# Kernel optimization log

Hardware: AMD Instinct MI355X
Metric: run time of the kernel (lower is better)

The kernel has to match this reference:

```python
import jax, jax.numpy as jnp
import numpy as np

V, E, HD, K = 100000, 128, 256, 9
B, T = 128, 512
H = HD // 2  # per-direction hidden size


def setup_inputs() -> dict:
    key = jax.random.key(0)
    ks = jax.random.split(key, 16)
    s = 0.1
    rn = lambda k, shape: jax.random.normal(k, shape, jnp.float32) * s
    sentences = jax.random.randint(ks[0], (B, T), 0, V, dtype=jnp.int32)
    lengths = jax.random.randint(ks[1], (B,), 1, T + 1, dtype=jnp.int32)
    return {
        'sentences': sentences,
        'lengths': lengths,
        'embed': rn(ks[2], (V, E)),
        'Wih_f': rn(ks[3], (4 * H, E)), 'Whh_f': rn(ks[4], (4 * H, H)),
        'bih_f': rn(ks[5], (4 * H,)), 'bhh_f': rn(ks[6], (4 * H,)),
        'Wih_b': rn(ks[7], (4 * H, E)), 'Whh_b': rn(ks[8], (4 * H, H)),
        'bih_b': rn(ks[9], (4 * H,)), 'bhh_b': rn(ks[10], (4 * H,)),
        'W_out': rn(ks[11], (K, HD)), 'b_out': rn(ks[12], (K,)),
        'start_t': rn(ks[13], (K,)), 'end_t': rn(ks[14], (K,)),
        'trans': rn(ks[15], (K, K)),
    }


def _lstm(x, mask, Wih, Whh, bih, bhh, reverse):
    # x: [B,T,E], mask: [B,T] bool. Replicates packed-sequence semantics:
    # state frozen and output zeroed at padding positions (padding is trailing,
    # so reverse=True starts fresh at each sequence's true end).
    Bv, Hv = x.shape[0], Whh.shape[1]
    bias = bih + bhh

    def step(carry, inp):
        h, c = carry
        x_t, m_t = inp  # [B,E], [B,1]
        gates = x_t @ Wih.T + h @ Whh.T + bias  # [B,4H]
        i, f, g, o = jnp.split(gates, 4, axis=-1)  # torch gate order i,f,g,o
        c_new = jax.nn.sigmoid(f) * c + jax.nn.sigmoid(i) * jnp.tanh(g)
        h_new = jax.nn.sigmoid(o) * jnp.tanh(c_new)
        h = jnp.where(m_t, h_new, h)
        c = jnp.where(m_t, c_new, c)
        return (h, c), h * m_t.astype(h.dtype)

    init = (jnp.zeros((Bv, Hv), x.dtype), jnp.zeros((Bv, Hv), x.dtype))
    xs = (jnp.swapaxes(x, 0, 1), jnp.swapaxes(mask, 0, 1)[..., None])
    _, hs = jax.lax.scan(step, init, xs, reverse=reverse)
    return jnp.swapaxes(hs, 0, 1)  # [B,T,H]


def _emissions(sentences, mask, embed, Wih_f, Whh_f, bih_f, bhh_f,
               Wih_b, Whh_b, bih_b, bhh_b, W_out, b_out):
    x = embed[sentences]  # [B,T,E] (dropout is identity at inference)
    hf = _lstm(x, mask, Wih_f, Whh_f, bih_f, bhh_f, reverse=False)
    hb = _lstm(x, mask, Wih_b, Whh_b, bih_b, bhh_b, reverse=True)
    h = jnp.concatenate([hf, hb], axis=-1)  # [B,T,2H]
    return jnp.einsum('btd,kd->btk', h, W_out) + b_out  # [B,T,K]


def _viterbi(em, mask, start_t, end_t, trans):
    # torchcrf-style batched Viterbi decode. em: [B,T,K], mask: [B,T] bool.
    Kv = em.shape[-1]
    ident = jnp.arange(Kv, dtype=jnp.int32)[None]  # identity backpointers for pads
    score0 = start_t[None] + em[:, 0]  # [B,K]

    def step(score, inp):
        em_t, m_t = inp  # [B,K], [B,1]
        cand = score[:, :, None] + trans[None] + em_t[:, None, :]  # [B,K_prev,K_cur]
        new_score = cand.max(axis=1)
        idx = cand.argmax(axis=1).astype(jnp.int32)  # [B,K]
        score = jnp.where(m_t, new_score, score)
        idx = jnp.where(m_t, idx, ident)
        return score, idx

    xs = (jnp.swapaxes(em[:, 1:], 0, 1), jnp.swapaxes(mask[:, 1:], 0, 1)[..., None])
    score, hist = jax.lax.scan(step, score0, xs)  # hist: [T-1,B,K]
    score = score + end_t[None]
    last_tag = jnp.argmax(score, axis=-1).astype(jnp.int32)  # [B]

    def back(tag, idx_t):
        prev = jnp.take_along_axis(idx_t, tag[:, None], axis=1)[:, 0]
        return prev, prev

    _, tags_prev = jax.lax.scan(back, last_tag, hist, reverse=True)  # [T-1,B]
    tags = jnp.swapaxes(jnp.concatenate([tags_prev, last_tag[None]], axis=0), 0, 1)
    return jnp.where(mask, tags, 0), score.max(axis=-1)


def reference(sentences, lengths, embed, Wih_f, Whh_f, bih_f, bhh_f,
              Wih_b, Whh_b, bih_b, bhh_b, W_out, b_out, start_t, end_t, trans):
    mask = jnp.arange(sentences.shape[1])[None] < lengths[:, None]  # [B,T]
    em = _emissions(sentences, mask, embed, Wih_f, Whh_f, bih_f, bhh_f,
                    Wih_b, Whh_b, bih_b, bhh_b, W_out, b_out)
    tags, _ = _viterbi(em, mask, start_t, end_t, trans)
    return tags  # [B,T] int32, padded positions set to 0
```

## Files before the change

### kernel.cpp

```cpp
#include <hip/hip_runtime.h>
#include <cmath>

#define B_  128
#define T_  512
#define E_  128
#define H_  128
#define G4  512
#define K_  9
#define HP  36

__global__ __launch_bounds__(256, 2)
void proj_gemm(const int* __restrict__ sent, const float* __restrict__ embed,
               const float* __restrict__ Wf, const float* __restrict__ Wb,
               const float* __restrict__ bif, const float* __restrict__ bhf,
               const float* __restrict__ bib, const float* __restrict__ bhb,
               float* __restrict__ proj, int t0f, int Tc)
{
  __shared__ __align__(16) float Al[128 * 64];
  __shared__ __align__(16) float Bl[128 * 64];
  const int tid   = threadIdx.x;
  const int ntile = blockIdx.x;
  const int mtile = blockIdx.y;
  const int tpb   = Tc >> 6;
  const int b     = mtile / tpb;
  const int toff  = (mtile - b * tpb) << 6;
  const int dir   = ntile >> 3;
  const int t0    = dir ? (T_ - t0f - Tc) : t0f;
  const float* __restrict__ W = dir ? Wb : Wf;
  const int n0 = (ntile & 7) << 6;

  {
    const int r  = tid & 63;
    const int kc = tid >> 6;
    const int t  = t0 + toff + r;
    const int vid = sent[b * T_ + t];
    const float* arow = embed + (size_t)vid * E_ + kc * 32;
    const float* brow = W + (size_t)(n0 + r) * E_ + kc * 32;
#pragma unroll
    for (int q = 0; q < 8; ++q) {
      float4 av = *(const float4*)(arow + q * 4);
      float4 bv = *(const float4*)(brow + q * 4);
      int k0 = kc * 32 + q * 4;
      Al[(k0 + 0) * 64 + r] = av.x; Al[(k0 + 1) * 64 + r] = av.y;
      Al[(k0 + 2) * 64 + r] = av.z; Al[(k0 + 3) * 64 + r] = av.w;
      Bl[(k0 + 0) * 64 + r] = bv.x; Bl[(k0 + 1) * 64 + r] = bv.y;
      Bl[(k0 + 2) * 64 + r] = bv.z; Bl[(k0 + 3) * 64 + r] = bv.w;
    }
  }
  __syncthreads();

  const int mg = tid & 15, ng = tid >> 4;
  float acc[4][4] = {};
#pragma unroll 8
  for (int k = 0; k < 128; ++k) {
    float4 a  = *(const float4*)&Al[k * 64 + mg * 4];
    float4 bb = *(const float4*)&Bl[k * 64 + ng * 4];
    acc[0][0] += a.x * bb.x; acc[0][1] += a.x * bb.y; acc[0][2] += a.x * bb.z; acc[0][3] += a.x * bb.w;
    acc[1][0] += a.y * bb.x; acc[1][1] += a.y * bb.y; acc[1][2] += a.y * bb.z; acc[1][3] += a.y * bb.w;
    acc[2][0] += a.z * bb.x; acc[2][1] += a.z * bb.y; acc[2][2] += a.z * bb.z; acc[2][3] += a.z * bb.w;
    acc[3][0] += a.w * bb.x; acc[3][1] += a.w * bb.y; acc[3][2] += a.w * bb.z; acc[3][3] += a.w * bb.w;
  }

  const float* bi = dir ? bib : bif;
  const float* bh = dir ? bhb : bhf;
  const int nl = ng * 4;
  float4 bias;
  bias.x = bi[n0 + nl + 0] + bh[n0 + nl + 0];
  bias.y = bi[n0 + nl + 1] + bh[n0 + nl + 1];
  bias.z = bi[n0 + nl + 2] + bh[n0 + nl + 2];
  bias.w = bi[n0 + nl + 3] + bh[n0 + nl + 3];
#pragma unroll
  for (int i = 0; i < 4; ++i) {
    const int tloc = toff + mg * 4 + i;
    float4 o;
    o.x = acc[i][0] + bias.x; o.y = acc[i][1] + bias.y;
    o.z = acc[i][2] + bias.z; o.w = acc[i][3] + bias.w;
    *(float4*)&proj[((size_t)(b * Tc + tloc)) * 1024 + dir * G4 + n0 + nl] = o;
  }
}

__device__ __forceinline__ float fast_rcp(float x) {
  return __builtin_amdgcn_rcpf(x);
}
__device__ __forceinline__ float fast_sig(float x) {
  return fast_rcp(1.f + __expf(-x));
}
__device__ __forceinline__ float fast_tanh(float x) {
  return 2.f * fast_rcp(1.f + __expf(-2.f * x)) - 1.f;
}

__global__ __launch_bounds__(1024)
void lstm_chunk(const float* __restrict__ proj,
                const float* __restrict__ Whf, const float* __restrict__ Whb,
                const int* __restrict__ lengths,
                float* __restrict__ hs,
                float* __restrict__ sh, float* __restrict__ sc,
                int t0f, int Tc, int first)
{
  const int dir = blockIdx.x;
  const int b   = blockIdx.y;
  const int tid = threadIdx.x;
  const int l   = tid & 63;
  const int wv  = tid >> 6;
  const int u   = wv * 8 + (l & 7);
  const int gp  = (l >> 3) & 1;
  const int kq  = l >> 4;
  const int rowA = u + (gp ? 256 : 0);
  const int rowB = rowA + 128;
  const float* __restrict__ Whh = dir ? Whb : Whf;
  __shared__ __align__(16) float h_hist[2][4 * HP];

  float wA[32], wB[32];
  {
    const float* wra = Whh + (size_t)rowA * H_ + kq * 32;
    const float* wrb = Whh + (size_t)rowB * H_ + kq * 32;
#pragma unroll
    for (int k = 0; k < 32; k += 4) {
      float4 va = *(const float4*)(wra + k);
      float4 vb = *(const float4*)(wrb + k);
      wA[k] = va.x; wA[k + 1] = va.y; wA[k + 2] = va.z; wA[k + 3] = va.w;
      wB[k] = vb.x; wB[k + 1] = vb.y; wB[k + 2] = vb.z; wB[k + 3] = vb.w;
    }
  }
#pragma unroll
  for (int k = 0; k < 32; ++k) {
    asm volatile("" : "+v"(wA[k]));
    asm volatile("" : "+v"(wB[k]));
  }

  const int len = lengths[b];
  const int t0  = dir ? (T_ - t0f - Tc) : t0f;
  const float fgp = (float)gp;
  const float kf  = 1.f + fgp;
  float c = 0.f, h_reg = 0.f;
  if (!first) {
    c     = sc[(dir * B_ + b) * H_ + u];
    h_reg = sh[(dir * B_ + b) * H_ + u];
  }
  if (l < 8) h_hist[1][(u >> 5) * HP + (u & 31)] = h_reg;
  __syncthreads();

  const float* projpA = proj + (size_t)b * Tc * 1024 + dir * G4 + rowA;
  const float* projpB = projpA + 128;
  const int tc00 = dir ? (Tc - 1) : 0;
  float pvA = projpA[(size_t)tc00 * 1024];
  float pvB = projpB[(size_t)tc00 * 1024];

  for (int s = 0; s < Tc; ++s) {
    const int tc = dir ? (Tc - 1 - s) : s;
    const int t  = t0 + tc;
    float nvA = 0.f, nvB = 0.f;
    if (s + 1 < Tc) {
      const int tcn = dir ? (Tc - 2 - s) : (s + 1);
      nvA = projpA[(size_t)tcn * 1024];
      nvB = projpB[(size_t)tcn * 1024];
    }
    const float* hp = &h_hist[(s + 1) & 1][kq * HP];
    float a0 = 0.f, a1 = 0.f, a2 = 0.f, a3 = 0.f;
#pragma unroll
    for (int k4 = 0; k4 < 8; ++k4) {
      float4 h4 = *(const float4*)&hp[k4 * 4];
      a0 += wA[4 * k4 + 0] * h4.x; a1 += wA[4 * k4 + 1] * h4.y;
      a0 += wA[4 * k4 + 2] * h4.z; a1 += wA[4 * k4 + 3] * h4.w;
      a2 += wB[4 * k4 + 0] * h4.x; a3 += wB[4 * k4 + 1] * h4.y;
      a2 += wB[4 * k4 + 2] * h4.z; a3 += wB[4 * k4 + 3] * h4.w;
    }
    float sA = a0 + a1;
    sA += __shfl_xor(sA, 16); sA += __shfl_xor(sA, 32); sA += pvA;
    float sB = a2 + a3;
    sB += __shfl_xor(sB, 16); sB += __shfl_xor(sB, 32); sB += pvB;
    const float gA = kf * fast_rcp(1.f + __expf(-kf * sA)) - fgp;
    const float gB = fast_sig(sB);
    const float xA = __shfl_xor(gA, 8);
    const float xB = __shfl_xor(gB, 8);
    const float gi = gp ? xA : gA;
    const float gf = gp ? xB : gB;
    const float gg = gp ? gA : xA;
    const float go = gp ? gB : xB;
    const float cn = gf * c + gi * gg;
    const float hn = go * fast_tanh(cn);
    const bool  m  = (t < len);
    c     = m ? cn : c;
    h_reg = m ? hn : h_reg;
    if (l < 8) {
      h_hist[s & 1][(u >> 5) * HP + (u & 31)] = h_reg;
      hs[(size_t)(b * T_ + t) * 256 + dir * H_ + u] = m ? hn : 0.f;
    }
    __syncthreads();
    pvA = nvA; pvB = nvB;
  }
  if (l < 8) {
    sh[(dir * B_ + b) * H_ + u] = h_reg;
    sc[(dir * B_ + b) * H_ + u] = c;
  }
}

__global__ __launch_bounds__(256)
void emis_kernel(const float* __restrict__ hs, const float* __restrict__ Wout,
                 const float* __restrict__ bout, float* __restrict__ em)
{
  __shared__ __align__(16) float Wl[K_ * 256];
  const int tid = threadIdx.x;
  for (int i = tid; i < K_ * 256; i += 256) Wl[i] = Wout[i];
  __syncthreads();
  const int m = blockIdx.x * 256 + tid;
  const float* h = hs + (size_t)m * 256;
  float acc[K_] = {};
#pragma unroll 4
  for (int kk = 0; kk < 64; ++kk) {
    float4 h4 = *(const float4*)(h + kk * 4);
#pragma unroll
    for (int k9 = 0; k9 < K_; ++k9) {
      float4 w4 = *(const float4*)&Wl[k9 * 256 + kk * 4];
      acc[k9] += h4.x * w4.x + h4.y * w4.y + h4.z * w4.z + h4.w * w4.w;
    }
  }
#pragma unroll
  for (int k9 = 0; k9 < K_; ++k9) em[(size_t)m * K_ + k9] = acc[k9] + bout[k9];
}

__global__ __launch_bounds__(64)
void viterbi_kernel(const float* __restrict__ em, const int* __restrict__ lengths,
                    const float* __restrict__ st, const float* __restrict__ en,
                    const float* __restrict__ trans, int* __restrict__ tags)
{
  const int b    = blockIdx.x;
  const int lane = threadIdx.x;
  __shared__ unsigned char hist[(T_ - 1) * 16];
  const int len = lengths[b];
  float tr[K_];
#pragma unroll
  for (int j = 0; j < K_; ++j) tr[j] = (lane < K_) ? trans[j * K_ + lane] : 0.f;
  float s = (lane < K_) ? st[lane] + em[(size_t)(b * T_) * K_ + lane] : -1e30f;
  for (int t = 1; t < len; ++t) {
    float best = -1e30f; int bj = 0;
#pragma unroll
    for (int j = 0; j < K_; ++j) {
      float v = __shfl(s, j) + tr[j];
      if (v > best) { best = v; bj = j; }
    }
    if (lane < K_) {
      s = best + em[(size_t)(b * T_ + t) * K_ + lane];
      hist[(t - 1) * 16 + lane] = (unsigned char)bj;
    }
  }
  float fs = (lane < K_) ? s + en[lane] : -1e30f;
  float best = -1e30f; int last = 0;
#pragma unroll
  for (int j = 0; j < K_; ++j) {
    float v = __shfl(fs, j);
    if (v > best) { best = v; last = j; }
  }
  __syncthreads();
  if (lane == 0) {
    int tag = last;
    tags[b * T_ + len - 1] = tag;
    for (int t = len - 2; t >= 0; --t) {
      tag = hist[t * 16 + tag];
      tags[b * T_ + t] = tag;
    }
  }
  for (int t = len + lane; t < T_; t += 64) tags[b * T_ + t] = 0;
}

extern "C" void kernel_launch(void* const* d_in, const int* in_sizes, int n_in,
                              void* d_out, int out_size, void* d_ws, size_t ws_size,
                              hipStream_t stream)
{
  const int*   sent  = (const int*)d_in[0];
  const int*   lens  = (const int*)d_in[1];
  const float* embed = (const float*)d_in[2];
  const float* Wif   = (const float*)d_in[3];
  const float* Whf   = (const float*)d_in[4];
  const float* bif   = (const float*)d_in[5];
  const float* bhf   = (const float*)d_in[6];
  const float* Wib   = (const float*)d_in[7];
  const float* Whb   = (const float*)d_in[8];
  const float* bib   = (const float*)d_in[9];
  const float* bhb   = (const float*)d_in[10];
  const float* Wout  = (const float*)d_in[11];
  const float* bout  = (const float*)d_in[12];
  const float* stt   = (const float*)d_in[13];
  const float* ent   = (const float*)d_in[14];
  const float* trans = (const float*)d_in[15];
  int* tags = (int*)d_out;

  float* ws   = (float*)d_ws;
  float* hs   = ws;
  float* em   = hs + (size_t)B_ * T_ * 256;
  float* sh   = em + (size_t)B_ * T_ * K_;
  float* sc   = sh + (size_t)2 * B_ * H_;
  float* proj = sc + (size_t)2 * B_ * H_;
  const size_t fixed_bytes = (size_t)(proj - ws) * sizeof(float);

  int Tc = 512;
  while (Tc > 64 && fixed_bytes + (size_t)B_ * Tc * 1024 * sizeof(float) > ws_size)
    Tc >>= 1;

  const int nch = T_ / Tc;
  for (int c2 = 0; c2 < nch; ++c2) {
    const int t0f = c2 * Tc;
    dim3 g1(16, B_ * (Tc >> 6));
    hipLaunchKernelGGL(proj_gemm, g1, dim3(256), 0, stream,
                       sent, embed, Wif, Wib, bif, bhf, bib, bhb, proj, t0f, Tc);
    dim3 g2(2, B_);
    hipLaunchKernelGGL(lstm_chunk, g2, dim3(1024), 0, stream,
                       proj, Whf, Whb, lens, hs, sh, sc, t0f, Tc, (int)(c2 == 0));
  }
  hipLaunchKernelGGL(emis_kernel, dim3((B_ * T_) / 256), dim3(256), 0, stream,
                     hs, Wout, bout, em);
  hipLaunchKernelGGL(viterbi_kernel, dim3(B_), dim3(64), 0, stream,
                     em, lens, stt, ent, trans, tags);
}
```

Baseline: 920.1 us.

## Give each LSTM thread all four gates of one unit, halving block size

The recurrent LSTM kernel now uses 512 threads per block. Each thread holds all four gate weight rows (i, f, g, o) for one hidden unit, 128 registers of weights, instead of two gate rows split across lane pairs. This removes the cross-lane shuffle exchange of gate activations and the two-gate-per-lane arithmetic trick. It allows two blocks per CU and halves the threads taking part in each per-step barrier. In exchange each thread does twice the FMAs per step and register pressure rises, which risks lower occupancy or spills.

Result: faster. 882.8 us (-4.1%).

```diff
diff --git a/kernel.cpp b/kernel.cpp
--- a/kernel.cpp
+++ b/kernel.cpp
@@ -89,7 +89,7 @@
   return 2.f * fast_rcp(1.f + __expf(-2.f * x)) - 1.f;
 }
 
-__global__ __launch_bounds__(1024)
+__global__ __launch_bounds__(512, 2)
 void lstm_chunk(const float* __restrict__ proj,
                 const float* __restrict__ Whf, const float* __restrict__ Whb,
                 const int* __restrict__ lengths,
@@ -102,94 +102,95 @@
   const int tid = threadIdx.x;
   const int l   = tid & 63;
   const int wv  = tid >> 6;
-  const int u   = wv * 8 + (l & 7);
-  const int gp  = (l >> 3) & 1;
+  const int u   = wv * 16 + (l & 15);
   const int kq  = l >> 4;
-  const int rowA = u + (gp ? 256 : 0);
-  const int rowB = rowA + 128;
   const float* __restrict__ Whh = dir ? Whb : Whf;
   __shared__ __align__(16) float h_hist[2][4 * HP];
 
-  float wA[32], wB[32];
+  float wI[32], wF[32], wG[32], wO[32];
   {
-    const float* wra = Whh + (size_t)rowA * H_ + kq * 32;
-    const float* wrb = Whh + (size_t)rowB * H_ + kq * 32;
+    const float* wi = Whh + (size_t)(u)       * H_ + kq * 32;
+    const float* wf = Whh + (size_t)(u + 128) * H_ + kq * 32;
+    const float* wg = Whh + (size_t)(u + 256) * H_ + kq * 32;
+    const float* wo = Whh + (size_t)(u + 384) * H_ + kq * 32;
 #pragma unroll
     for (int k = 0; k < 32; k += 4) {
-      float4 va = *(const float4*)(wra + k);
-      float4 vb = *(const float4*)(wrb + k);
-      wA[k] = va.x; wA[k + 1] = va.y; wA[k + 2] = va.z; wA[k + 3] = va.w;
-      wB[k] = vb.x; wB[k + 1] = vb.y; wB[k + 2] = vb.z; wB[k + 3] = vb.w;
+      float4 vi = *(const float4*)(wi + k);
+      float4 vf = *(const float4*)(wf + k);
+      float4 vg = *(const float4*)(wg + k);
+      float4 vo = *(const float4*)(wo + k);
+      wI[k] = vi.x; wI[k + 1] = vi.y; wI[k + 2] = vi.z; wI[k + 3] = vi.w;
+      wF[k] = vf.x; wF[k + 1] = vf.y; wF[k + 2] = vf.z; wF[k + 3] = vf.w;
+      wG[k] = vg.x; wG[k + 1] = vg.y; wG[k + 2] = vg.z; wG[k + 3] = vg.w;
+      wO[k] = vo.x; wO[k + 1] = vo.y; wO[k + 2] = vo.z; wO[k + 3] = vo.w;
     }
   }
 #pragma unroll
   for (int k = 0; k < 32; ++k) {
-    asm volatile("" : "+v"(wA[k]));
-    asm volatile("" : "+v"(wB[k]));
+    asm volatile("" : "+v"(wI[k])); asm volatile("" : "+v"(wF[k]));
+    asm volatile("" : "+v"(wG[k])); asm volatile("" : "+v"(wO[k]));
   }
 
   const int len = lengths[b];
   const int t0  = dir ? (T_ - t0f - Tc) : t0f;
-  const float fgp = (float)gp;
-  const float kf  = 1.f + fgp;
   float c = 0.f, h_reg = 0.f;
   if (!first) {
     c     = sc[(dir * B_ + b) * H_ + u];
     h_reg = sh[(dir * B_ + b) * H_ + u];
   }
-  if (l < 8) h_hist[1][(u >> 5) * HP + (u & 31)] = h_reg;
+  if (l < 16) h_hist[1][(u >> 5) * HP + (u & 31)] = h_reg;
   __syncthreads();
 
-  const float* projpA = proj + (size_t)b * Tc * 1024 + dir * G4 + rowA;
-  const float* projpB = projpA + 128;
-  const int tc00 = dir ? (Tc - 1) : 0;
-  float pvA = projpA[(size_t)tc00 * 1024];
-  float pvB = projpB[(size_t)tc00 * 1024];
+  const long stp = dir ? -1024 : 1024;
+  const float* pp = proj + (size_t)b * Tc * 1024 + dir * G4 + u
+                         + (size_t)(dir ? (Tc - 1) : 0) * 1024;
+  float pvI = pp[0], pvF = pp[128], pvG = pp[256], pvO = pp[384];
 
   for (int s = 0; s < Tc; ++s) {
     const int tc = dir ? (Tc - 1 - s) : s;
     const int t  = t0 + tc;
-    float nvA = 0.f, nvB = 0.f;
+    float nI = 0.f, nF = 0.f, nG = 0.f, nO = 0.f;
     if (s + 1 < Tc) {
-      const int tcn = dir ? (Tc - 2 - s) : (s + 1);
-      nvA = projpA[(size_t)tcn * 1024];
-      nvB = projpB[(size_t)tcn * 1024];
+      const float* np = pp + stp;
+      nI = np[0]; nF = np[128]; nG = np[256]; nO = np[384];
     }
     const float* hp = &h_hist[(s + 1) & 1][kq * HP];
-    float a0 = 0.f, a1 = 0.f, a2 = 0.f, a3 = 0.f;
+    float aI0 = 0.f, aI1 = 0.f, aF0 = 0.f, aF1 = 0.f;
+    float aG0 = 0.f, aG1 = 0.f, aO0 = 0.f, aO1 = 0.f;
 #pragma unroll
     for (int k4 = 0; k4 < 8; ++k4) {
       float4 h4 = *(const float4*)&hp[k4 * 4];
-      a0 += wA[4 * k4 + 0] * h4.x; a1 += wA[4 * k4 + 1] * h4.y;
-      a0 += wA[4 * k4 + 2] * h4.z; a1 += wA[4 * k4 + 3] * h4.w;
-      a2 += wB[4 * k4 + 0] * h4.x; a3 += wB[4 * k4 + 1] * h4.y;
-      a2 += wB[4 * k4 + 2] * h4.z; a3 += wB[4 * k4 + 3] * h4.w;
-    }
-    float sA = a0 + a1;
-    sA += __shfl_xor(sA, 16); sA += __shfl_xor(sA, 32); sA += pvA;
-    float sB = a2 + a3;
-    sB += __shfl_xor(sB, 16); sB += __shfl_xor(sB, 32); sB += pvB;
-    const float gA = kf * fast_rcp(1.f + __expf(-kf * sA)) - fgp;
-    const float gB = fast_sig(sB);
-    const float xA = __shfl_xor(gA, 8);
-    const float xB = __shfl_xor(gB, 8);
-    const float gi = gp ? xA : gA;
-    const float gf = gp ? xB : gB;
-    const float gg = gp ? gA : xA;
-    const float go = gp ? gB : xB;
+      aI0 += wI[4 * k4 + 0] * h4.x; aI1 += wI[4 * k4 + 1] * h4.y;
+      aI0 += wI[4 * k4 + 2] * h4.z; aI1 += wI[4 * k4 + 3] * h4.w;
+      aF0 += wF[4 * k4 + 0] * h4.x; aF1 += wF[4 * k4 + 1] * h4.y;
+      aF0 += wF[4 * k4 + 2] * h4.z; aF1 += wF[4 * k4 + 3] * h4.w;
+      aG0 += wG[4 * k4 + 0] * h4.x; aG1 += wG[4 * k4 + 1] * h4.y;
+      aG0 += wG[4 * k4 + 2] * h4.z; aG1 += wG[4 * k4 + 3] * h4.w;
+      aO0 += wO[4 * k4 + 0] * h4.x; aO1 += wO[4 * k4 + 1] * h4.y;
+      aO0 += wO[4 * k4 + 2] * h4.z; aO1 += wO[4 * k4 + 3] * h4.w;
+    }
+    float sI = aI0 + aI1; sI += __shfl_xor(sI, 16); sI += __shfl_xor(sI, 32);
+    float sF = aF0 + aF1; sF += __shfl_xor(sF, 16); sF += __shfl_xor(sF, 32);
+    float sG = aG0 + aG1; sG += __shfl_xor(sG, 16); sG += __shfl_xor(sG, 32);
+    float sO = aO0 + aO1; sO += __shfl_xor(sO, 16); sO += __shfl_xor(sO, 32);
+    const float gi = fast_sig(sI + pvI);
+    const float gf = fast_sig(sF + pvF);
+    const float gg = fast_tanh(sG + pvG);
+    const float go = fast_sig(sO + pvO);
     const float cn = gf * c + gi * gg;
     const float hn = go * fast_tanh(cn);
     const bool  m  = (t < len);
     c     = m ? cn : c;
     h_reg = m ? hn : h_reg;
-    if (l < 8) {
+    if (l < 16) {
       h_hist[s & 1][(u >> 5) * HP + (u & 31)] = h_reg;
       hs[(size_t)(b * T_ + t) * 256 + dir * H_ + u] = m ? hn : 0.f;
     }
     __syncthreads();
-    pvA = nvA; pvB = nvB;
-  }
-  if (l < 8) {
+    pp += stp;
+    pvI = nI; pvF = nF; pvG = nG; pvO = nO;
+  }
+  if (l < 16) {
     sh[(dir * B_ + b) * H_ + u] = h_reg;
     sc[(dir * B_ + b) * H_ + u] = c;
   }
@@ -304,7 +305,7 @@
     hipLaunchKernelGGL(proj_gemm, g1, dim3(256), 0, stream,
                        sent, embed, Wif, Wib, bif, bhf, bib, bhb, proj, t0f, Tc);
     dim3 g2(2, B_);
-    hipLaunchKernelGGL(lstm_chunk, g2, dim3(1024), 0, stream,
+    hipLaunchKernelGGL(lstm_chunk, g2, dim3(512), 0, stream,
                        proj, Whf, Whb, lens, hs, sh, sc, t0f, Tc, (int)(c2 == 0));
   }
   hipLaunchKernelGGL(emis_kernel, dim3((B_ * T_) / 256), dim3(256), 0, stream,
```
